# Kernel tuning notes

Measured on AMD Instinct MI355X. Metric: run time of the kernel, lower is better.

## Reference

```python
import jax, jax.numpy as jnp
import numpy as np

BN_EPS = 1e-5

def conv1x1(x, w, b):
    # x: [B,C,H,W], w: [O,C], b: [O] -> [B,O,H,W]
    return jnp.einsum('bchw,oc->bohw', x, w) + b[None, :, None, None]

def setup_inputs() -> dict:
    key = jax.random.key(0)
    ks = jax.random.split(key, 12)
    B, C, H, W = 16, 512, 64, 32
    Ch = C // 2  # hidden_channel
    s = 0.02
    return {
        'x':       jax.random.normal(ks[0], (B, C, H, W), jnp.float32),
        'theta_w': jax.random.normal(ks[1], (Ch, C), jnp.float32) * s,
        'theta_b': jax.random.normal(ks[2], (Ch,), jnp.float32) * s,
        'phi_w':   jax.random.normal(ks[3], (Ch, C), jnp.float32) * s,
        'phi_b':   jax.random.normal(ks[4], (Ch,), jnp.float32) * s,
        'g_w':     jax.random.normal(ks[5], (Ch, C), jnp.float32) * s,
        'g_b':     jax.random.normal(ks[6], (Ch,), jnp.float32) * s,
        'W_w':     jax.random.normal(ks[7], (C, Ch), jnp.float32) * s,
        'W_b':     jax.random.normal(ks[8], (C,), jnp.float32) * s,
        'bn_gamma': 1.0 + jax.random.normal(ks[9], (C,), jnp.float32) * 0.1,
        'bn_beta':  jax.random.normal(ks[10], (C,), jnp.float32) * 0.1,
    }

def reference(x, theta_w, theta_b, phi_w, phi_b, g_w, g_b, W_w, W_b, bn_gamma, bn_beta):
    B, C, H, Wd = x.shape
    N = H * Wd
    Ch = theta_w.shape[0]
    # 1x1 conv projections, flattened over spatial dims
    th = conv1x1(x, theta_w, theta_b).reshape(B, Ch, N)  # theta: [B,Ch,N]
    ph = conv1x1(x, phi_w, phi_b).reshape(B, Ch, N)      # phi:   [B,Ch,N]
    gv = conv1x1(x, g_w, g_b).reshape(B, Ch, N)          # g:     [B,Ch,N]
    # dense affinity (no softmax), normalized by N, as in the original
    f = jnp.einsum('bcn,bcm->bnm', th, ph) / N           # [B,N,N]
    y = jnp.einsum('bnm,bcm->bcn', f, gv).reshape(B, Ch, H, Wd)
    # W: 1x1 conv + BatchNorm2d (training-mode batch statistics, biased var)
    w = conv1x1(y, W_w, W_b)                             # [B,C,H,W]
    mean = w.mean(axis=(0, 2, 3), keepdims=True)
    var = w.var(axis=(0, 2, 3), keepdims=True)
    wn = (w - mean) * jax.lax.rsqrt(var + BN_EPS)
    wn = wn * bn_gamma[None, :, None, None] + bn_beta[None, :, None, None]
    return wn + x
```

## Files before the change

### kernel.cpp

```cpp
#include <hip/hip_runtime.h>

typedef __bf16 bf16x8 __attribute__((ext_vector_type(8)));
typedef float floatx4 __attribute__((ext_vector_type(4)));

#define DEVI __device__ __forceinline__

DEVI unsigned short f2bf(float f) {
  union { float f; unsigned u; } v; v.f = f;
  unsigned r = v.u + 0x7FFFu + ((v.u >> 16) & 1u);
  return (unsigned short)(r >> 16);
}

DEVI void gload_lds16(const void* g, void* l) {
  __builtin_amdgcn_global_load_lds((const __attribute__((address_space(1))) void*)g,
                                   (__attribute__((address_space(3))) void*)l,
                                   16, 0, 0);
}

__global__ __launch_bounds__(256) void k_prep(
    const float* __restrict__ phi_w, const float* __restrict__ g_w,
    const float* __restrict__ theta_w, const float* __restrict__ W_w,
    const float* __restrict__ phi_b, const float* __restrict__ g_b,
    unsigned short* __restrict__ wpg, unsigned short* __restrict__ thw,
    unsigned short* __restrict__ ww, float* __restrict__ pgbias) {
  const int T0 = 512 * 512, T1 = T0 + 256 * 512, T2 = T1 + 512 * 256, T3 = T2 + 512;
  for (int i = blockIdx.x * 256 + threadIdx.x; i < T3; i += gridDim.x * 256) {
    if (i < T0) {
      int o = i >> 9, c = i & 511;
      float v = (o < 256) ? phi_w[o * 512 + c] : g_w[(o - 256) * 512 + c];
      wpg[i] = f2bf(v);
    } else if (i < T1) {
      int j = i - T0; thw[j] = f2bf(theta_w[j]);
    } else if (i < T2) {
      int j = i - T1; ww[j] = f2bf(W_w[j]);
    } else {
      int o = i - T2; pgbias[o] = (o < 256) ? phi_b[o] : g_b[o - 256];
    }
  }
}

__global__ __launch_bounds__(256) void k_transpose(const float* __restrict__ x,
                                                   unsigned short* __restrict__ xt) {
  __shared__ float tile[64][65];
  const int b = blockIdx.z, c0 = blockIdx.y * 64, n0 = blockIdx.x * 64;
  const int t = threadIdx.x;
  const float* xb = x + (size_t)b * 512 * 2048;
#pragma unroll
  for (int i = 0; i < 16; ++i) {
    int lin = i * 256 + t;
    int lc = lin >> 6, ln = lin & 63;
    tile[lc][ln] = xb[(size_t)(c0 + lc) * 2048 + (n0 + ln)];
  }
  __syncthreads();
  unsigned short* xtb = xt + (size_t)b * 2048 * 512;
#pragma unroll
  for (int i = 0; i < 16; ++i) {
    int lin = i * 256 + t;
    int ln = lin >> 6, lc = lin & 63;
    xtb[(size_t)(n0 + ln) * 512 + (c0 + lc)] = f2bf(tile[lc][ln]);
  }
}

template <int BM, int BN, int EPI>
__global__ __launch_bounds__(256) void k_gemm_abt(
    const unsigned short* __restrict__ A, const unsigned short* __restrict__ B,
    unsigned short* __restrict__ C, int M, int N, int K,
    size_t sA, size_t sB, size_t sC,
    const float* __restrict__ bias, float scale) {
  constexpr int WM = BM / 2, WN = BN / 2;
  constexpr int FM = WM / 16, FN = WN / 16;
  __shared__ __align__(16) __bf16 At[BM * 32];
  __shared__ __align__(16) __bf16 Bt[BN * 32];
  const int t = threadIdx.x;
  const int z = blockIdx.z;
  const int row0 = blockIdx.y * BM;
  const int col0 = blockIdx.x * BN;
  const unsigned short* Az = A + (size_t)z * sA;
  const unsigned short* Bz = B + (size_t)z * sB;
  unsigned short* Cz = C + (size_t)z * sC;

  const int w = t >> 6, lane = t & 63;
  const int l16 = lane & 15, lq = lane >> 4;
  const int wrow0 = (w >> 1) * WM, wcol0 = (w & 1) * WN;

  floatx4 acc[FM][FN];
#pragma unroll
  for (int m = 0; m < FM; ++m)
#pragma unroll
    for (int n = 0; n < FN; ++n) acc[m][n] = (floatx4){0.f, 0.f, 0.f, 0.f};

  const int kt_end = K >> 5;
  for (int kt = 0; kt < kt_end; ++kt) {
    __syncthreads();
#pragma unroll
    for (int i = 0; i < BM * 4 / 256; ++i) {
      int ch = i * 256 + t;
      int r = ch >> 2, kq = ch & 3;
      gload_lds16(Az + (size_t)(row0 + r) * K + (kt << 5) + (kq << 3), &At[ch * 8]);
    }
#pragma unroll
    for (int i = 0; i < BN * 4 / 256; ++i) {
      int ch = i * 256 + t;
      int r = ch >> 2, kq = ch & 3;
      gload_lds16(Bz + (size_t)(col0 + r) * K + (kt << 5) + (kq << 3), &Bt[ch * 8]);
    }
    __syncthreads();

    bf16x8 af[FM], bq[FN];
#pragma unroll
    for (int m = 0; m < FM; ++m)
      af[m] = *(const bf16x8*)&At[(wrow0 + m * 16 + l16) * 32 + lq * 8];
#pragma unroll
    for (int n = 0; n < FN; ++n)
      bq[n] = *(const bf16x8*)&Bt[(wcol0 + n * 16 + l16) * 32 + lq * 8];
#pragma unroll
    for (int m = 0; m < FM; ++m)
#pragma unroll
      for (int n = 0; n < FN; ++n)
        acc[m][n] = __builtin_amdgcn_mfma_f32_16x16x32_bf16(af[m], bq[n], acc[m][n], 0, 0, 0);
  }

#pragma unroll
  for (int m = 0; m < FM; ++m)
#pragma unroll
    for (int n = 0; n < FN; ++n)
#pragma unroll
      for (int r = 0; r < 4; ++r) {
        int gr = row0 + wrow0 + m * 16 + lq * 4 + r;
        int gc = col0 + wcol0 + n * 16 + l16;
        float v = acc[m][n][r] * scale;
        if (EPI == 1) v += bias[gr];
        if (EPI == 2) v += bias[gc];
        Cz[(size_t)gr * N + gc] = f2bf(v);
      }
}

__global__ __launch_bounds__(256) void k_bnstats(const unsigned short* __restrict__ w,
                                                 const float* __restrict__ gamma,
                                                 const float* __restrict__ beta,
                                                 float* __restrict__ scale,
                                                 float* __restrict__ shift) {
  const int c = blockIdx.x, t = threadIdx.x;
  float s = 0.f, ss = 0.f;
  for (int b = 0; b < 16; ++b) {
    const unsigned short* p = w + ((size_t)b * 512 + c) * 2048 + t * 8;
    uint4 v = *(const uint4*)p;
    unsigned u[4] = {v.x, v.y, v.z, v.w};
#pragma unroll
    for (int j = 0; j < 4; ++j) {
      union { unsigned q; float f; } a, bb;
      a.q = u[j] << 16;
      bb.q = u[j] & 0xFFFF0000u;
      s += a.f + bb.f;
      ss += a.f * a.f + bb.f * bb.f;
    }
  }
#pragma unroll
  for (int off = 32; off; off >>= 1) {
    s += __shfl_down(s, off);
    ss += __shfl_down(ss, off);
  }
  __shared__ float ls[4], lss[4];
  if ((t & 63) == 0) { ls[t >> 6] = s; lss[t >> 6] = ss; }
  __syncthreads();
  if (t == 0) {
    float S = ls[0] + ls[1] + ls[2] + ls[3];
    float SS = lss[0] + lss[1] + lss[2] + lss[3];
    const float inv = 1.f / 32768.f;
    float mean = S * inv;
    float var = SS * inv - mean * mean;
    float rs = rsqrtf(var + 1e-5f);
    float sc = gamma[c] * rs;
    scale[c] = sc;
    shift[c] = beta[c] - mean * sc;
  }
}

__global__ __launch_bounds__(256) void k_final(const unsigned short* __restrict__ w,
                                               const float* __restrict__ x,
                                               const float* __restrict__ scale,
                                               const float* __restrict__ shift,
                                               float* __restrict__ out) {
  const size_t total4 = (size_t)16 * 512 * 2048 / 4;
  size_t stride = (size_t)gridDim.x * 256;
  for (size_t i = (size_t)blockIdx.x * 256 + threadIdx.x; i < total4; i += stride) {
    size_t e = i * 4;
    int c = (int)((e >> 11) & 511);
    float sc = scale[c], sh = shift[c];
    uint2 wv = *(const uint2*)(w + e);
    float4 xv = *(const float4*)(x + e);
    float4 o;
    union { unsigned q; float f; } a;
    a.q = wv.x << 16;          o.x = a.f * sc + sh + xv.x;
    a.q = wv.x & 0xFFFF0000u;  o.y = a.f * sc + sh + xv.y;
    a.q = wv.y << 16;          o.z = a.f * sc + sh + xv.z;
    a.q = wv.y & 0xFFFF0000u;  o.w = a.f * sc + sh + xv.w;
    *(float4*)(out + e) = o;
  }
}

extern "C" void kernel_launch(void* const* d_in, const int* in_sizes, int n_in,
                              void* d_out, int out_size, void* d_ws, size_t ws_size,
                              hipStream_t stream) {
  const float* x       = (const float*)d_in[0];
  const float* theta_w = (const float*)d_in[1];
  const float* theta_b = (const float*)d_in[2];
  const float* phi_w   = (const float*)d_in[3];
  const float* phi_b   = (const float*)d_in[4];
  const float* g_w     = (const float*)d_in[5];
  const float* g_b     = (const float*)d_in[6];
  const float* W_w     = (const float*)d_in[7];
  const float* W_b     = (const float*)d_in[8];
  const float* gamma   = (const float*)d_in[9];
  const float* beta    = (const float*)d_in[10];
  float* out = (float*)d_out;

  char* ws = (char*)d_ws;
  size_t off = 0;
  auto alloc = [&](size_t bytes) {
    char* p = ws + off;
    off = (off + bytes + 255) & ~(size_t)255;
    return p;
  };
  unsigned short* xt    = (unsigned short*)alloc((size_t)16 * 2048 * 512 * 2);
  unsigned short* phg   = (unsigned short*)alloc((size_t)16 * 512 * 2048 * 2);
  unsigned short* tht   = (unsigned short*)alloc((size_t)16 * 2048 * 256 * 2);
  unsigned short* amat  = (unsigned short*)alloc((size_t)16 * 256 * 256 * 2);
  unsigned short* mmat  = (unsigned short*)alloc((size_t)16 * 512 * 256 * 2);
  unsigned short* wbuf  = (unsigned short*)alloc((size_t)16 * 512 * 2048 * 2);
  unsigned short* wpg   = (unsigned short*)alloc((size_t)512 * 512 * 2);
  unsigned short* thw   = (unsigned short*)alloc((size_t)256 * 512 * 2);
  unsigned short* ww    = (unsigned short*)alloc((size_t)512 * 256 * 2);
  float* pgbias         = (float*)alloc(512 * 4);
  float* scale          = (float*)alloc(512 * 4);
  float* shift          = (float*)alloc(512 * 4);
  (void)ws_size; (void)in_sizes; (void)n_in; (void)out_size;

  const size_t sXT = (size_t)2048 * 512;
  const size_t sPG = (size_t)512 * 2048;
  const size_t sTH = (size_t)2048 * 256;
  const size_t sAM = (size_t)256 * 256;
  const size_t sMM = (size_t)512 * 256;
  const size_t sW  = (size_t)512 * 2048;

  k_prep<<<1024, 256, 0, stream>>>(phi_w, g_w, theta_w, W_w, phi_b, g_b, wpg, thw, ww, pgbias);
  k_transpose<<<dim3(32, 8, 16), 256, 0, stream>>>(x, xt);

  k_gemm_abt<128, 128, 1><<<dim3(16, 4, 16), 256, 0, stream>>>(
      wpg, xt, phg, 512, 2048, 512, 0, sXT, sPG, pgbias, 1.f);
  k_gemm_abt<128, 128, 2><<<dim3(2, 16, 16), 256, 0, stream>>>(
      xt, thw, tht, 2048, 256, 512, sXT, 0, sTH, theta_b, 1.f);
  k_gemm_abt<64, 64, 0><<<dim3(4, 4, 16), 256, 0, stream>>>(
      phg, phg + (size_t)256 * 2048, amat, 256, 256, 2048, sPG, sPG, sAM, nullptr, 1.f);
  k_gemm_abt<64, 64, 0><<<dim3(4, 8, 16), 256, 0, stream>>>(
      ww, amat, mmat, 512, 256, 256, 0, sAM, sMM, nullptr, 1.f / 2048.f);
  k_gemm_abt<128, 128, 1><<<dim3(16, 4, 16), 256, 0, stream>>>(
      mmat, tht, wbuf, 512, 2048, 256, sMM, sTH, sW, W_b, 1.f);

  k_bnstats<<<512, 256, 0, stream>>>(wbuf, gamma, beta, scale, shift);
  k_final<<<4096, 256, 0, stream>>>(wbuf, x, scale, shift, out);
}
```

Measured before the change: 265.2 us.

## Fuse prep into transpose, split-K affinity GEMM, fuse BN stats into GEMM epilogue

Folds the weight-prep kernel into the transpose launch as an extra z-slice. Replaces the low-occupancy phi·g^T GEMM with a 256x256-tile split-K kernel that accumulates fp32 partials atomically, and converts them to bf16 in the following GEMM's loader. Computes BatchNorm sums in the final GEMM epilogue with shuffles and atomics, which removes the separate stats pass over wbuf. Also remaps block IDs so batches are interleaved across blocks. The cost is atomic contention, an extra memset, and a larger fp32 intermediate.

```diff
diff --git a/kernel.cpp b/kernel.cpp
--- a/kernel.cpp
+++ b/kernel.cpp
@@ -17,33 +17,34 @@
                                    16, 0, 0);
 }
 
-__global__ __launch_bounds__(256) void k_prep(
+__global__ __launch_bounds__(256) void k_transpose(
+    const float* __restrict__ x, unsigned short* __restrict__ xt,
     const float* __restrict__ phi_w, const float* __restrict__ g_w,
     const float* __restrict__ theta_w, const float* __restrict__ W_w,
     const float* __restrict__ phi_b, const float* __restrict__ g_b,
     unsigned short* __restrict__ wpg, unsigned short* __restrict__ thw,
     unsigned short* __restrict__ ww, float* __restrict__ pgbias) {
-  const int T0 = 512 * 512, T1 = T0 + 256 * 512, T2 = T1 + 512 * 256, T3 = T2 + 512;
-  for (int i = blockIdx.x * 256 + threadIdx.x; i < T3; i += gridDim.x * 256) {
-    if (i < T0) {
-      int o = i >> 9, c = i & 511;
-      float v = (o < 256) ? phi_w[o * 512 + c] : g_w[(o - 256) * 512 + c];
-      wpg[i] = f2bf(v);
-    } else if (i < T1) {
-      int j = i - T0; thw[j] = f2bf(theta_w[j]);
-    } else if (i < T2) {
-      int j = i - T1; ww[j] = f2bf(W_w[j]);
-    } else {
-      int o = i - T2; pgbias[o] = (o < 256) ? phi_b[o] : g_b[o - 256];
-    }
-  }
-}
-
-__global__ __launch_bounds__(256) void k_transpose(const float* __restrict__ x,
-                                                   unsigned short* __restrict__ xt) {
+  const int t = threadIdx.x;
+  if (blockIdx.z == 16) {
+    const int T0 = 512 * 512, T1 = T0 + 256 * 512, T2 = T1 + 512 * 256, T3 = T2 + 512;
+    int base = (blockIdx.y * 32 + blockIdx.x) * 256 + t;
+    for (int i = base; i < T3; i += 65536) {
+      if (i < T0) {
+        int o = i >> 9, c = i & 511;
+        float v = (o < 256) ? phi_w[o * 512 + c] : g_w[(o - 256) * 512 + c];
+        wpg[i] = f2bf(v);
+      } else if (i < T1) {
+        int j = i - T0; thw[j] = f2bf(theta_w[j]);
+      } else if (i < T2) {
+        int j = i - T1; ww[j] = f2bf(W_w[j]);
+      } else {
+        int o = i - T2; pgbias[o] = (o < 256) ? phi_b[o] : g_b[o - 256];
+      }
+    }
+    return;
+  }
   __shared__ float tile[64][65];
   const int b = blockIdx.z, c0 = blockIdx.y * 64, n0 = blockIdx.x * 64;
-  const int t = threadIdx.x;
   const float* xb = x + (size_t)b * 512 * 2048;
 #pragma unroll
   for (int i = 0; i < 16; ++i) {
@@ -61,23 +62,25 @@
   }
 }
 
-template <int BM, int BN, int EPI>
-__global__ __launch_bounds__(256) void k_gemm_abt(
+template <int BM, int BN, int EPI, bool BNS, int T, int NTX>
+__global__ __launch_bounds__(256) void k_gemm(
     const unsigned short* __restrict__ A, const unsigned short* __restrict__ B,
-    unsigned short* __restrict__ C, int M, int N, int K,
+    unsigned short* __restrict__ C, int N, int K,
     size_t sA, size_t sB, size_t sC,
-    const float* __restrict__ bias, float scale) {
+    const float* __restrict__ bias, float scale, float* __restrict__ bnsum) {
   constexpr int WM = BM / 2, WN = BN / 2;
   constexpr int FM = WM / 16, FN = WN / 16;
   __shared__ __align__(16) __bf16 At[BM * 32];
   __shared__ __align__(16) __bf16 Bt[BN * 32];
   const int t = threadIdx.x;
-  const int z = blockIdx.z;
-  const int row0 = blockIdx.y * BM;
-  const int col0 = blockIdx.x * BN;
-  const unsigned short* Az = A + (size_t)z * sA;
-  const unsigned short* Bz = B + (size_t)z * sB;
-  unsigned short* Cz = C + (size_t)z * sC;
+  const int lid = blockIdx.x;
+  const int b = (lid & 7) + 8 * ((lid >> 3) / T);
+  const int tt = (lid >> 3) % T;
+  const int col0 = (tt % NTX) * BN;
+  const int row0 = (tt / NTX) * BM;
+  const unsigned short* Az = A + (size_t)b * sA;
+  const unsigned short* Bz = B + (size_t)b * sB;
+  unsigned short* Cz = C + (size_t)b * sC;
 
   const int w = t >> 6, lane = t & 63;
   const int l16 = lane & 15, lq = lane >> 4;
@@ -120,73 +123,205 @@
         acc[m][n] = __builtin_amdgcn_mfma_f32_16x16x32_bf16(af[m], bq[n], acc[m][n], 0, 0, 0);
   }
 
+  float sv[FM][4], ssv[FM][4];
+  if (BNS) {
+#pragma unroll
+    for (int m = 0; m < FM; ++m)
+#pragma unroll
+      for (int r = 0; r < 4; ++r) { sv[m][r] = 0.f; ssv[m][r] = 0.f; }
+  }
 #pragma unroll
   for (int m = 0; m < FM; ++m)
 #pragma unroll
-    for (int n = 0; n < FN; ++n)
+    for (int n = 0; n < FN; ++n) {
+      int gc = col0 + wcol0 + n * 16 + l16;
+      float bc = (EPI == 2) ? bias[gc] : 0.f;
+#pragma unroll
+      for (int r = 0; r < 4; ++r) {
+        int gr = row0 + wrow0 + m * 16 + lq * 4 + r;
+        float v = acc[m][n][r] * scale;
+        if (EPI == 1) v += bias[gr];
+        if (EPI == 2) v += bc;
+        if (BNS) { sv[m][r] += v; ssv[m][r] += v * v; }
+        Cz[(size_t)gr * N + gc] = f2bf(v);
+      }
+    }
+  if (BNS) {
+#pragma unroll
+    for (int m = 0; m < FM; ++m)
+#pragma unroll
+      for (int r = 0; r < 4; ++r) {
+        float s = sv[m][r], ss = ssv[m][r];
+        s += __shfl_xor(s, 1); ss += __shfl_xor(ss, 1);
+        s += __shfl_xor(s, 2); ss += __shfl_xor(ss, 2);
+        s += __shfl_xor(s, 4); ss += __shfl_xor(ss, 4);
+        s += __shfl_xor(s, 8); ss += __shfl_xor(ss, 8);
+        if (l16 == 0) {
+          int gr = row0 + wrow0 + m * 16 + lq * 4 + r;
+          unsafeAtomicAdd(&bnsum[gr], s);
+          unsafeAtomicAdd(&bnsum[512 + gr], ss);
+        }
+      }
+  }
+}
+
+__global__ __launch_bounds__(512) void k_gemm_splitk(const unsigned short* __restrict__ phg,
+                                                     float* __restrict__ amatf) {
+  __shared__ __align__(16) __bf16 At[256 * 32];
+  __shared__ __align__(16) __bf16 Bt[256 * 32];
+  const int t = threadIdx.x;
+  const int lid = blockIdx.x;
+  const int b = (lid & 7) + 8 * (lid >> 5);
+  const int split = (lid >> 3) & 3;
+  const size_t sPG = (size_t)512 * 2048;
+  const unsigned short* Az = phg + (size_t)b * sPG;
+  const unsigned short* Bz = Az + (size_t)256 * 2048;
+  const int w = t >> 6, lane = t & 63;
+  const int l16 = lane & 15, lq = lane >> 4;
+  const int wrow0 = (w >> 2) * 128, wcol0 = (w & 3) * 64;
+
+  floatx4 acc[8][4];
+#pragma unroll
+  for (int m = 0; m < 8; ++m)
+#pragma unroll
+    for (int n = 0; n < 4; ++n) acc[m][n] = (floatx4){0.f, 0.f, 0.f, 0.f};
+
+  const int kt0 = split * 16;
+  for (int kk = 0; kk < 16; ++kk) {
+    const int kt = kt0 + kk;
+    __syncthreads();
+#pragma unroll
+    for (int i = 0; i < 2; ++i) {
+      int ch = i * 512 + t;
+      int r = ch >> 2, kq = ch & 3;
+      gload_lds16(Az + (size_t)r * 2048 + (kt << 5) + (kq << 3), &At[ch * 8]);
+    }
+#pragma unroll
+    for (int i = 0; i < 2; ++i) {
+      int ch = i * 512 + t;
+      int r = ch >> 2, kq = ch & 3;
+      gload_lds16(Bz + (size_t)r * 2048 + (kt << 5) + (kq << 3), &Bt[ch * 8]);
+    }
+    __syncthreads();
+    bf16x8 af[8], bq[4];
+#pragma unroll
+    for (int m = 0; m < 8; ++m)
+      af[m] = *(const bf16x8*)&At[(wrow0 + m * 16 + l16) * 32 + lq * 8];
+#pragma unroll
+    for (int n = 0; n < 4; ++n)
+      bq[n] = *(const bf16x8*)&Bt[(wcol0 + n * 16 + l16) * 32 + lq * 8];
+#pragma unroll
+    for (int m = 0; m < 8; ++m)
+#pragma unroll
+      for (int n = 0; n < 4; ++n)
+        acc[m][n] = __builtin_amdgcn_mfma_f32_16x16x32_bf16(af[m], bq[n], acc[m][n], 0, 0, 0);
+  }
+  float* out = amatf + (size_t)b * 256 * 256;
+#pragma unroll
+  for (int m = 0; m < 8; ++m)
+#pragma unroll
+    for (int n = 0; n < 4; ++n)
+#pragma unroll
+      for (int r = 0; r < 4; ++r) {
+        int gr = wrow0 + m * 16 + lq * 4 + r;
+        int gc = wcol0 + n * 16 + l16;
+        unsafeAtomicAdd(&out[gr * 256 + gc], acc[m][n][r]);
+      }
+}
+
+__global__ __launch_bounds__(256) void k_gemm_f32b(const unsigned short* __restrict__ ww,
+                                                   const float* __restrict__ amatf,
+                                                   unsigned short* __restrict__ mmat) {
+  __shared__ __align__(16) __bf16 At[64 * 32];
+  __shared__ __align__(16) __bf16 Bt[64 * 32];
+  const int t = threadIdx.x;
+  const int lid = blockIdx.x;
+  const int b = (lid & 7) + 8 * ((lid >> 3) / 32);
+  const int tt = (lid >> 3) % 32;
+  const int col0 = (tt & 3) * 64;
+  const int row0 = (tt >> 2) * 64;
+  const float* Bz = amatf + (size_t)b * 256 * 256;
+  const int w = t >> 6, lane = t & 63;
+  const int l16 = lane & 15, lq = lane >> 4;
+  const int wrow0 = (w >> 1) * 32, wcol0 = (w & 1) * 32;
+
+  floatx4 acc[2][2];
+#pragma unroll
+  for (int m = 0; m < 2; ++m)
+#pragma unroll
+    for (int n = 0; n < 2; ++n) acc[m][n] = (floatx4){0.f, 0.f, 0.f, 0.f};
+
+  for (int kt = 0; kt < 8; ++kt) {
+    __syncthreads();
+    {
+      int r = t >> 2, kq = t & 3;
+      gload_lds16(ww + (size_t)(row0 + r) * 256 + (kt << 5) + (kq << 3), &At[t * 8]);
+    }
+    {
+      int r = t >> 2, kq = t & 3;
+      const float* src = Bz + (size_t)(col0 + r) * 256 + (kt << 5) + (kq << 3);
+      float4 a = *(const float4*)src;
+      float4 c = *(const float4*)(src + 4);
+      union { unsigned short s[8]; bf16x8 v; } pk;
+      pk.s[0] = f2bf(a.x); pk.s[1] = f2bf(a.y); pk.s[2] = f2bf(a.z); pk.s[3] = f2bf(a.w);
+      pk.s[4] = f2bf(c.x); pk.s[5] = f2bf(c.y); pk.s[6] = f2bf(c.z); pk.s[7] = f2bf(c.w);
+      *(bf16x8*)&Bt[t * 8] = pk.v;
+    }
+    __syncthreads();
+    bf16x8 af[2], bq[2];
+#pragma unroll
+    for (int m = 0; m < 2; ++m)
+      af[m] = *(const bf16x8*)&At[(wrow0 + m * 16 + l16) * 32 + lq * 8];
+#pragma unroll
+    for (int n = 0; n < 2; ++n)
+      bq[n] = *(const bf16x8*)&Bt[(wcol0 + n * 16 + l16) * 32 + lq * 8];
+#pragma unroll
+    for (int m = 0; m < 2; ++m)
+#pragma unroll
+      for (int n = 0; n < 2; ++n)
+        acc[m][n] = __builtin_amdgcn_mfma_f32_16x16x32_bf16(af[m], bq[n], acc[m][n], 0, 0, 0);
+  }
+  unsigned short* Cz = mmat + (size_t)b * 512 * 256;
+  const float scale = 1.f / 2048.f;
+#pragma unroll
+  for (int m = 0; m < 2; ++m)
+#pragma unroll
+    for (int n = 0; n < 2; ++n)
 #pragma unroll
       for (int r = 0; r < 4; ++r) {
         int gr = row0 + wrow0 + m * 16 + lq * 4 + r;
         int gc = col0 + wcol0 + n * 16 + l16;
-        float v = acc[m][n][r] * scale;
-        if (EPI == 1) v += bias[gr];
-        if (EPI == 2) v += bias[gc];
-        Cz[(size_t)gr * N + gc] = f2bf(v);
-      }
-}
-
-__global__ __launch_bounds__(256) void k_bnstats(const unsigned short* __restrict__ w,
-                                                 const float* __restrict__ gamma,
-                                                 const float* __restrict__ beta,
-                                                 float* __restrict__ scale,
-                                                 float* __restrict__ shift) {
-  const int c = blockIdx.x, t = threadIdx.x;
-  float s = 0.f, ss = 0.f;
-  for (int b = 0; b < 16; ++b) {
-    const unsigned short* p = w + ((size_t)b * 512 + c) * 2048 + t * 8;
-    uint4 v = *(const uint4*)p;
-    unsigned u[4] = {v.x, v.y, v.z, v.w};
-#pragma unroll
-    for (int j = 0; j < 4; ++j) {
-      union { unsigned q; float f; } a, bb;
-      a.q = u[j] << 16;
-      bb.q = u[j] & 0xFFFF0000u;
-      s += a.f + bb.f;
-      ss += a.f * a.f + bb.f * bb.f;
-    }
-  }
-#pragma unroll
-  for (int off = 32; off; off >>= 1) {
-    s += __shfl_down(s, off);
-    ss += __shfl_down(ss, off);
-  }
-  __shared__ float ls[4], lss[4];
-  if ((t & 63) == 0) { ls[t >> 6] = s; lss[t >> 6] = ss; }
-  __syncthreads();
-  if (t == 0) {
-    float S = ls[0] + ls[1] + ls[2] + ls[3];
-    float SS = lss[0] + lss[1] + lss[2] + lss[3];
+        Cz[(size_t)gr * 256 + gc] = f2bf(acc[m][n][r] * scale);
+      }
+}
+
+__global__ __launch_bounds__(256) void k_final(const unsigned short* __restrict__ w,
+                                               const float* __restrict__ x,
+                                               const float* __restrict__ bnsum,
+                                               const float* __restrict__ gamma,
+                                               const float* __restrict__ beta,
+                                               float* __restrict__ out) {
+  __shared__ float ssc[512], ssh[512];
+  const int t = threadIdx.x;
+#pragma unroll
+  for (int i = 0; i < 2; ++i) {
+    int c = t + i * 256;
+    float S = bnsum[c], SS = bnsum[512 + c];
     const float inv = 1.f / 32768.f;
     float mean = S * inv;
     float var = SS * inv - mean * mean;
     float rs = rsqrtf(var + 1e-5f);
     float sc = gamma[c] * rs;
-    scale[c] = sc;
-    shift[c] = beta[c] - mean * sc;
-  }
-}
-
-__global__ __launch_bounds__(256) void k_final(const unsigned short* __restrict__ w,
-                                               const float* __restrict__ x,
-                                               const float* __restrict__ scale,
-                                               const float* __restrict__ shift,
-                                               float* __restrict__ out) {
+    ssc[c] = sc;
+    ssh[c] = beta[c] - mean * sc;
+  }
+  __syncthreads();
   const size_t total4 = (size_t)16 * 512 * 2048 / 4;
   size_t stride = (size_t)gridDim.x * 256;
-  for (size_t i = (size_t)blockIdx.x * 256 + threadIdx.x; i < total4; i += stride) {
+  for (size_t i = (size_t)blockIdx.x * 256 + t; i < total4; i += stride) {
     size_t e = i * 4;
     int c = (int)((e >> 11) & 511);
-    float sc = scale[c], sh = shift[c];
+    float sc = ssc[c], sh = ssh[c];
     uint2 wv = *(const uint2*)(w + e);
     float4 xv = *(const float4*)(x + e);
     float4 o;
@@ -225,38 +360,35 @@
   unsigned short* xt    = (unsigned short*)alloc((size_t)16 * 2048 * 512 * 2);
   unsigned short* phg   = (unsigned short*)alloc((size_t)16 * 512 * 2048 * 2);
   unsigned short* tht   = (unsigned short*)alloc((size_t)16 * 2048 * 256 * 2);
-  unsigned short* amat  = (unsigned short*)alloc((size_t)16 * 256 * 256 * 2);
+  float*          amatf = (float*)alloc((size_t)16 * 256 * 256 * 4);
+  float*          bnsum = (float*)alloc(1024 * 4);
   unsigned short* mmat  = (unsigned short*)alloc((size_t)16 * 512 * 256 * 2);
   unsigned short* wbuf  = (unsigned short*)alloc((size_t)16 * 512 * 2048 * 2);
   unsigned short* wpg   = (unsigned short*)alloc((size_t)512 * 512 * 2);
   unsigned short* thw   = (unsigned short*)alloc((size_t)256 * 512 * 2);
   unsigned short* ww    = (unsigned short*)alloc((size_t)512 * 256 * 2);
   float* pgbias         = (float*)alloc(512 * 4);
-  float* scale          = (float*)alloc(512 * 4);
-  float* shift          = (float*)alloc(512 * 4);
   (void)ws_size; (void)in_sizes; (void)n_in; (void)out_size;
 
   const size_t sXT = (size_t)2048 * 512;
   const size_t sPG = (size_t)512 * 2048;
   const size_t sTH = (size_t)2048 * 256;
-  const size_t sAM = (size_t)256 * 256;
   const size_t sMM = (size_t)512 * 256;
   const size_t sW  = (size_t)512 * 2048;
 
-  k_prep<<<1024, 256, 0, stream>>>(phi_w, g_w, theta_w, W_w, phi_b, g_b, wpg, thw, ww, pgbias);
-  k_transpose<<<dim3(32, 8, 16), 256, 0, stream>>>(x, xt);
-
-  k_gemm_abt<128, 128, 1><<<dim3(16, 4, 16), 256, 0, stream>>>(
-      wpg, xt, phg, 512, 2048, 512, 0, sXT, sPG, pgbias, 1.f);
-  k_gemm_abt<128, 128, 2><<<dim3(2, 16, 16), 256, 0, stream>>>(
-      xt, thw, tht, 2048, 256, 512, sXT, 0, sTH, theta_b, 1.f);
-  k_gemm_abt<64, 64, 0><<<dim3(4, 4, 16), 256, 0, stream>>>(
-      phg, phg + (size_t)256 * 2048, amat, 256, 256, 2048, sPG, sPG, sAM, nullptr, 1.f);
-  k_gemm_abt<64, 64, 0><<<dim3(4, 8, 16), 256, 0, stream>>>(
-      ww, amat, mmat, 512, 256, 256, 0, sAM, sMM, nullptr, 1.f / 2048.f);
-  k_gemm_abt<128, 128, 1><<<dim3(16, 4, 16), 256, 0, stream>>>(
-      mmat, tht, wbuf, 512, 2048, 256, sMM, sTH, sW, W_b, 1.f);
-
-  k_bnstats<<<512, 256, 0, stream>>>(wbuf, gamma, beta, scale, shift);
-  k_final<<<4096, 256, 0, stream>>>(wbuf, x, scale, shift, out);
-}
+  hipMemsetAsync(amatf, 0, (size_t)16 * 256 * 256 * 4 + 1024 * 4, stream);
+
+  k_transpose<<<dim3(32, 8, 17), 256, 0, stream>>>(x, xt, phi_w, g_w, theta_w, W_w,
+                                                   phi_b, g_b, wpg, thw, ww, pgbias);
+
+  k_gemm<128, 128, 1, false, 64, 16><<<1024, 256, 0, stream>>>(
+      wpg, xt, phg, 2048, 512, 0, sXT, sPG, pgbias, 1.f, nullptr);
+  k_gemm<128, 128, 2, false, 32, 2><<<512, 256, 0, stream>>>(
+      xt, thw, tht, 256, 512, sXT, 0, sTH, theta_b, 1.f, nullptr);
+  k_gemm_splitk<<<64, 512, 0, stream>>>(phg, amatf);
+  k_gemm_f32b<<<512, 256, 0, stream>>>(ww, amatf, mmat);
+  k_gemm<128, 128, 1, true, 64, 16><<<1024, 256, 0, stream>>>(
+      mmat, tht, wbuf, 2048, 256, sMM, sTH, sW, W_b, 1.f, bnsum);
+
+  k_final<<<4096, 256, 0, stream>>>(wbuf, x, bnsum, gamma, beta, out);
+}
```

Measured after the change: 325.5 us. 1.23x slower.
